# Kernel tuning notes

Hardware: AMD Instinct MI355X
Metric: run time of the kernel (lower is better)

Reference implementation:

```python
import jax, jax.numpy as jnp
import numpy as np

INPUT_DIM = 23
LSTM_DIM = 128
HID = 64            # lstm_dim // 2 per direction
MAMBA_DIM = 128
D_INNER = 256       # expand * d_model
D_STATE = 64
D_CONV = 4
DT_RANK = 8         # ceil(d_model / 16)
NUM_LAYERS = 4
SEQ, BATCH = 2048, 4


def setup_inputs() -> dict:
    key = jax.random.key(0)
    ks = iter(jax.random.split(key, 40))
    def rn(shape, s=0.05):
        return jax.random.normal(next(ks), shape, jnp.float32) * s
    inp = {}
    inp["x"] = jax.random.normal(next(ks), (SEQ, BATCH, INPUT_DIM), jnp.float32)
    # 4-layer bidirectional LSTM params (PyTorch layout: W_ih [4H, in], W_hh [4H, H])
    inp["lstm_Wih0"] = rn((2, 4 * HID, INPUT_DIM))
    inp["lstm_WihR"] = rn((NUM_LAYERS - 1, 2, 4 * HID, LSTM_DIM))
    inp["lstm_Whh"] = rn((NUM_LAYERS, 2, 4 * HID, HID))
    inp["lstm_bih"] = rn((NUM_LAYERS, 2, 4 * HID))
    inp["lstm_bhh"] = rn((NUM_LAYERS, 2, 4 * HID))
    # mamba input projection Linear(input_dim, mamba_dim)
    inp["mproj_W"] = rn((MAMBA_DIM, INPUT_DIM))
    inp["mproj_b"] = rn((MAMBA_DIM,))
    # Mamba block params
    inp["in_proj_W"] = rn((2 * D_INNER, MAMBA_DIM))
    inp["conv_w"] = rn((D_INNER, 1, D_CONV))
    inp["conv_b"] = rn((D_INNER,))
    inp["x_proj_W"] = rn((DT_RANK + 2 * D_STATE, D_INNER))
    inp["dt_W"] = rn((D_INNER, DT_RANK))
    inp["dt_b"] = rn((D_INNER,))
    inp["A_log"] = jnp.tile(jnp.log(jnp.arange(1.0, D_STATE + 1.0, dtype=jnp.float32))[None, :], (D_INNER, 1))
    inp["D_skip"] = jnp.ones((D_INNER,), jnp.float32)
    inp["out_proj_W"] = rn((MAMBA_DIM, D_INNER))
    # gate: LayerNorm(lstm_dim + mamba_dim) -> Linear(-> 1) -> sigmoid
    inp["gate_ln_w"] = jnp.ones((LSTM_DIM + MAMBA_DIM,), jnp.float32)
    inp["gate_ln_b"] = jnp.zeros((LSTM_DIM + MAMBA_DIM,), jnp.float32)
    inp["gate_W"] = rn((1, LSTM_DIM + MAMBA_DIM))
    inp["gate_b"] = rn((1,))
    return inp


def _lstm_dir(x, Wih, Whh, b, reverse):
    # x: [L, B, in]; one direction of one LSTM layer. PyTorch gate order i,f,g,o.
    h0 = jnp.zeros((x.shape[1], Whh.shape[1]), x.dtype)
    def step(carry, xt):
        h, c = carry
        g = xt @ Wih.T + h @ Whh.T + b
        i, f, gg, o = jnp.split(g, 4, axis=-1)
        c = jax.nn.sigmoid(f) * c + jax.nn.sigmoid(i) * jnp.tanh(gg)
        h = jax.nn.sigmoid(o) * jnp.tanh(c)
        return (h, c), h
    _, hs = jax.lax.scan(step, (h0, h0), x, reverse=reverse)
    return hs


def _lstm(x, Wih0, WihR, Whh, bih, bhh):
    out = x
    for l in range(NUM_LAYERS):
        Wf = Wih0[0] if l == 0 else WihR[l - 1, 0]
        Wb = Wih0[1] if l == 0 else WihR[l - 1, 1]
        hf = _lstm_dir(out, Wf, Whh[l, 0], bih[l, 0] + bhh[l, 0], False)
        hb = _lstm_dir(out, Wb, Whh[l, 1], bih[l, 1] + bhh[l, 1], True)
        out = jnp.concatenate([hf, hb], axis=-1)  # [L, B, 2H]
    return out


def _mamba(x, in_proj_W, conv_w, conv_b, x_proj_W, dt_W, dt_b, A_log, D_skip, out_proj_W):
    # x: [L, B, d_model]; time axis = 0
    L = x.shape[0]
    xi, z = jnp.split(x @ in_proj_W.T, 2, axis=-1)          # [L,B,d_inner] each
    xp = jnp.pad(xi, ((D_CONV - 1, 0), (0, 0), (0, 0)))      # causal depthwise conv
    conv = conv_b + sum(xp[k:k + L] * conv_w[:, 0, k] for k in range(D_CONV))
    xc = jax.nn.silu(conv)
    dbc = xc @ x_proj_W.T                                    # [L,B,dt_rank+2*d_state]
    dt, Bm, Cm = jnp.split(dbc, [DT_RANK, DT_RANK + D_STATE], axis=-1)
    dt = jax.nn.softplus(dt @ dt_W.T + dt_b)                 # [L,B,d_inner]
    A = -jnp.exp(A_log)                                      # [d_inner,d_state]
    def step(h, inp):
        dt_t, B_t, C_t, x_t = inp
        h = jnp.exp(dt_t[..., None] * A) * h + dt_t[..., None] * B_t[:, None, :] * x_t[..., None]
        return h, jnp.einsum('bds,bs->bd', h, C_t)
    h0 = jnp.zeros((x.shape[1], D_INNER, D_STATE), x.dtype)
    _, ys = jax.lax.scan(step, h0, (dt, Bm, Cm, xc))          # ys: [L,B,d_inner]
    y = (ys + xc * D_skip) * jax.nn.silu(z)
    return y @ out_proj_W.T                                   # [L,B,d_model]


def _forward(x, lstm_Wih0, lstm_WihR, lstm_Whh, lstm_bih, lstm_bhh, mproj_W, mproj_b,
             in_proj_W, conv_w, conv_b, x_proj_W, dt_W, dt_b, A_log, D_skip, out_proj_W,
             gate_ln_w, gate_ln_b, gate_W, gate_b):
    lstm_out = _lstm(x, lstm_Wih0, lstm_WihR, lstm_Whh, lstm_bih, lstm_bhh)  # [L,B,128]
    mamba_out = _mamba(x @ mproj_W.T + mproj_b, in_proj_W, conv_w, conv_b,
                       x_proj_W, dt_W, dt_b, A_log, D_skip, out_proj_W)      # [L,B,128]
    comb = jnp.concatenate([lstm_out, mamba_out], axis=-1)                   # [L,B,256]
    mu = comb.mean(-1, keepdims=True)
    var = comb.var(-1, keepdims=True)
    ln = (comb - mu) / jnp.sqrt(var + 1e-5) * gate_ln_w + gate_ln_b
    gate = jax.nn.sigmoid(ln @ gate_W.T + gate_b)                            # [L,B,1]
    return gate * lstm_out + (1.0 - gate) * mamba_out


def reference(x, lstm_Wih0, lstm_WihR, lstm_Whh, lstm_bih, lstm_bhh, mproj_W, mproj_b,
              in_proj_W, conv_w, conv_b, x_proj_W, dt_W, dt_b, A_log, D_skip, out_proj_W,
              gate_ln_w, gate_ln_b, gate_W, gate_b):
    return _forward(x, lstm_Wih0, lstm_WihR, lstm_Whh, lstm_bih, lstm_bhh, mproj_W, mproj_b,
                    in_proj_W, conv_w, conv_b, x_proj_W, dt_W, dt_b, A_log, D_skip, out_proj_W,
                    gate_ln_w, gate_ln_b, gate_W, gate_b)
```

## Files before the change

### kernel.cpp

```cpp
#include <hip/hip_runtime.h>

#define SEQ   2048
#define NM    8192

typedef __attribute__((ext_vector_type(4))) float f4;
typedef _Float16 f16x8 __attribute__((ext_vector_type(8)));

__device__ __forceinline__ float frcp(float x){ return __builtin_amdgcn_rcpf(x); }
__device__ __forceinline__ float sigm(float x){ return frcp(1.f + __expf(-x)); }
__device__ __forceinline__ float tanhf_(float x){ return 1.f - 2.f*frcp(__expf(2.f*x) + 1.f); }
__device__ __forceinline__ f4 mfma16h(f16x8 a, f16x8 b, f4 c){
  return __builtin_amdgcn_mfma_f32_16x16x32_f16(a, b, c, 0, 0, 0);
}
__device__ __forceinline__ void barrier_lds_only(){
  asm volatile("s_waitcnt lgkmcnt(0)\n\ts_barrier" ::: "memory");
}

__global__ __launch_bounds__(256) void gemm_k(
    const float* __restrict__ A, int lda,
    const float* __restrict__ W0, const float* __restrict__ W1, int Nhalf,
    const float* __restrict__ b0a, const float* __restrict__ b0b,
    const float* __restrict__ b1a, const float* __restrict__ b1b,
    float* __restrict__ out, int M, int N, int K, int mode)
{
  __shared__ alignas(16) float As[16][68];
  __shared__ alignas(16) float Ws[16][68];
  const int tid = threadIdx.x;
  const int tn = tid & 15, tm = tid >> 4;
  const int n0 = blockIdx.x * 64, m0 = blockIdx.y * 64;
  const int srow = tid >> 2, sk = (tid & 3) * 4;
  float acc[4][4] = {};
  for (int k0 = 0; k0 < K; k0 += 16) {
    const int am = m0 + srow;
    #pragma unroll
    for (int q = 0; q < 4; ++q) {
      int k = k0 + sk + q;
      As[sk + q][srow] = (k < K) ? A[(size_t)am * lda + k] : 0.f;
    }
    const int wn = n0 + srow;
    const float* Wp = W0; int nn = wn;
    if (W1 != nullptr && wn >= Nhalf) { Wp = W1; nn = wn - Nhalf; }
    #pragma unroll
    for (int q = 0; q < 4; ++q) {
      int k = k0 + sk + q;
      Ws[sk + q][srow] = (wn < N && k < K) ? Wp[(size_t)nn * K + k] : 0.f;
    }
    __syncthreads();
    #pragma unroll
    for (int k = 0; k < 16; ++k) {
      f4 a = *(const f4*)&As[k][tm*4];
      f4 w = *(const f4*)&Ws[k][tn*4];
      #pragma unroll
      for (int i = 0; i < 4; ++i)
        #pragma unroll
        for (int j = 0; j < 4; ++j) acc[i][j] += a[i]*w[j];
    }
    __syncthreads();
  }
  #pragma unroll
  for (int i = 0; i < 4; ++i) {
    #pragma unroll
    for (int j = 0; j < 4; ++j) {
      int m = m0 + tm*4 + i, n = n0 + tn*4 + j;
      if (n >= N) continue;
      float bias = 0.f;
      if (n < Nhalf) { if (b0a) bias += b0a[n]; if (b0b) bias += b0b[n]; }
      else { if (b1a) bias += b1a[n - Nhalf]; if (b1b) bias += b1b[n - Nhalf]; }
      float v = acc[i][j] + bias;
      if (mode == 2) {
        int dd = n >> 8, r = n & 255, t = m >> 2, b = m & 3;
        int gate = r >> 6, jj = r & 63;
        int tq = dd ? (SEQ - 1 - t) : t;
        out[((size_t)(dd*SEQ + tq) * 4 + b) * 256 + (jj << 2) + gate] = v;
      } else {
        out[(size_t)m * N + n] = v;
      }
    }
  }
}

__global__ __launch_bounds__(256) void wcomb_k(
    const float* __restrict__ inprojW, const float* __restrict__ mprojW,
    const float* __restrict__ mprojB, float* __restrict__ wc,
    float* __restrict__ bvec)
{
  int idx = blockIdx.x * 256 + threadIdx.x;
  if (idx >= 512 * 24) return;
  int n = idx / 24, c = idx % 24;
  const float* wi = inprojW + (size_t)n * 128;
  float s = 0.f;
  if (c < 23) {
    for (int k = 0; k < 128; ++k) s += wi[k] * mprojW[k*23 + c];
    wc[n*23 + c] = s;
  } else {
    for (int k = 0; k < 128; ++k) s += wi[k] * mprojB[k];
    bvec[n] = s;
  }
}

__global__ __launch_bounds__(256) void moutproj_k(
    const float* __restrict__ z, const float* __restrict__ ys,
    const float* __restrict__ xc, const float* __restrict__ Dsk,
    const float* __restrict__ Wp, float* __restrict__ out)
{
  __shared__ alignas(16) float As[16][68];
  __shared__ alignas(16) float Ws[16][68];
  const int tid = threadIdx.x;
  const int tn = tid & 15, tm = tid >> 4;
  const int n0 = blockIdx.x * 64, m0 = blockIdx.y * 64;
  const int srow = tid >> 2, sk = (tid & 3) * 4;
  float acc[4][4] = {};
  for (int k0 = 0; k0 < 256; k0 += 16) {
    #pragma unroll
    for (int q = 0; q < 4; ++q) {
      int k = k0 + sk + q;
      size_t idx = (size_t)(m0 + srow) * 256 + k;
      float zz = z[idx];
      As[sk + q][srow] = (ys[idx] + xc[idx]*Dsk[k]) * zz * sigm(zz);
      Ws[sk + q][srow] = Wp[(size_t)(n0 + srow) * 256 + k];
    }
    __syncthreads();
    #pragma unroll
    for (int k = 0; k < 16; ++k) {
      f4 a = *(const f4*)&As[k][tm*4];
      f4 w = *(const f4*)&Ws[k][tn*4];
      #pragma unroll
      for (int i = 0; i < 4; ++i)
        #pragma unroll
        for (int j = 0; j < 4; ++j) acc[i][j] += a[i]*w[j];
    }
    __syncthreads();
  }
  #pragma unroll
  for (int i = 0; i < 4; ++i)
    #pragma unroll
    for (int j = 0; j < 4; ++j)
      out[(size_t)(m0 + tm*4 + i) * 128 + n0 + tn*4 + j] = acc[i][j];
}

__global__ __launch_bounds__(256, 1) void fused_k(
    int stage,
    const float* __restrict__ G,
    const float* __restrict__ Whh,
    float* __restrict__ lout,
    const float* __restrict__ rA, int lda,
    const float* __restrict__ rW, const float* __restrict__ rbias,
    float* __restrict__ rout, int ldo, int N, int K,
    const float* __restrict__ dtW, const float* __restrict__ dtB,
    float* __restrict__ dtout,
    const float* __restrict__ mdbc, const float* __restrict__ mdtb,
    const float* __restrict__ mxc, const float* __restrict__ mAlog,
    float* __restrict__ mys)
{
  __shared__ alignas(16) _Float16 hb2[2][4][80];
  __shared__ float As[64][17];
  __shared__ float Ws[64][17];
  __shared__ float dtl[64][8];

  const int tid = threadIdx.x;

  if (blockIdx.x < 2) {
    __builtin_amdgcn_s_setprio(1);
    const int dir = blockIdx.x;
    const int w = tid >> 6, lane = tid & 63;
    const int q = lane >> 4, c = lane & 15;
    const int bb = c & 3, sel = c >> 2;
    const int mtile = 4*sel + w;
    const int jcol = mtile*4 + q;

    for (int i = tid; i < 2*4*80; i += 256) ((_Float16*)hb2)[i] = (_Float16)0.f;

    const float* Gd = G + (size_t)dir * SEQ * 1024;
    const float* Wd = Whh + dir * 256 * 64;

    f16x8 Wf[4][2];
    #pragma unroll
    for (int s2 = 0; s2 < 4; ++s2) {
      const int m = 4*s2 + w;
      const int orow = (c & 3)*64 + m*4 + (c >> 2);
      #pragma unroll
      for (int kt = 0; kt < 2; ++kt) {
        const float* src = Wd + orow*64 + kt*32 + q*8;
        #pragma unroll
        for (int e = 0; e < 8; ++e) Wf[s2][kt][e] = (_Float16)src[e];
      }
    }

    float cc = 0.f;

    auto loadG = [&](int t) -> f4 {
      return *(const f4*)(Gd + (((size_t)t*4 + bb) << 8) + mtile*16 + q*4);
    };
    f4 gp[8];
    #pragma unroll
    for (int i = 0; i < 8; ++i) gp[i] = loadG(i);
    __syncthreads();

    const bool sb0 = (sel & 1) != 0, sb1 = (sel & 2) != 0;

    auto step = [&](int t, f4 gv) {
      const int p0 = t & 1, p1 = p0 ^ 1;
      const f16x8 h0 = *(const f16x8*)&hb2[p0][bb][q*8];
      const f16x8 h1 = *(const f16x8*)&hb2[p0][bb][32 + q*8];
      const f4 zz = {0.f, 0.f, 0.f, 0.f};
      f4 a0 = mfma16h(Wf[0][0], h0, gv);
      f4 b0 = mfma16h(Wf[0][1], h1, zz);
      f4 a1 = mfma16h(Wf[1][0], h0, gv);
      f4 b1 = mfma16h(Wf[1][1], h1, zz);
      f4 a2 = mfma16h(Wf[2][0], h0, gv);
      f4 b2 = mfma16h(Wf[2][1], h1, zz);
      f4 a3 = mfma16h(Wf[3][0], h0, gv);
      f4 b3 = mfma16h(Wf[3][1], h1, zz);
      f4 g4;
      #pragma unroll
      for (int r = 0; r < 4; ++r) {
        float xlo01 = sb0 ? a1[r] : a0[r];
        float xlo23 = sb0 ? a3[r] : a2[r];
        float xlo   = sb1 ? xlo23 : xlo01;
        float xhi01 = sb0 ? b1[r] : b0[r];
        float xhi23 = sb0 ? b3[r] : b2[r];
        float xhi   = sb1 ? xhi23 : xhi01;
        g4[r] = xlo + xhi;
      }
      cc = sigm(g4[1])*cc + sigm(g4[0])*tanhf_(g4[2]);
      const float hh = sigm(g4[3])*tanhf_(cc);
      hb2[p1][bb][jcol] = (_Float16)hh;
      const int to = dir ? (SEQ-1 - t) : t;
      lout[((size_t)to*4 + bb)*128 + dir*64 + jcol] = hh;
      barrier_lds_only();
    };

    for (int t0 = 0; t0 < SEQ; t0 += 8) {
      #pragma unroll
      for (int i = 0; i < 8; ++i) {
        step(t0 + i, gp[i]);
        if (t0 + 8 + i < SEQ) gp[i] = loadG(t0 + 8 + i);
      }
    }
    return;
  }

  int rb = blockIdx.x - 2;

  if (stage == 1) {
    int idx = rb*256 + tid;
    int d = idx & 255, m2 = idx >> 8;
    int t = m2 >> 2, b = m2 & 3;
    float s = rbias[d];
    #pragma unroll
    for (int k = 0; k < 4; ++k) {
      int tt = t - 3 + k;
      if (tt >= 0) s += rA[(size_t)((tt*4 + b) << 8) + d] * rW[d*4 + k];
    }
    rout[idx] = s * sigm(s);
    return;
  }

  if (stage == 3) {
    const int wid = rb*4 + (tid >> 6);
    const int lane = tid & 63;
    const int b = wid >> 8, d = wid & 255;
    const float Av = -__expf(mAlog[d*64 + lane]);
    const float* pB  = mdbc + (size_t)b*136 + 8 + lane;
    const float* pC  = mdbc + (size_t)b*136 + 72 + lane;
    const float* pdt = mdtb + (size_t)b*256 + d;
    const float* px  = mxc  + (size_t)b*256 + d;
    float* py = mys + (size_t)b*256 + d;
    float h = 0.f;
    float Bv = pB[0], Cv = pC[0], dtv = pdt[0], xv = px[0];
    #pragma unroll 2
    for (int t = 0; t < SEQ; ++t) {
      float Bn = 0.f, Cn = 0.f, dtn = 0.f, xn = 0.f;
      if (t + 1 < SEQ) {
        size_t od = (size_t)(t+1) * 544;
        size_t ox = (size_t)(t+1) * 1024;
        Bn = pB[od]; Cn = pC[od]; dtn = pdt[ox]; xn = px[ox];
      }
      float a = __expf(dtv * Av);
      h = a*h + (dtv*xv)*Bv;
      float p = h * Cv;
      #pragma unroll
      for (int mm = 1; mm < 64; mm <<= 1) p += __shfl_xor(p, mm, 64);
      if (lane == 0) py[(size_t)t * 1024] = p;
      Bv = Bn; Cv = Cn; dtv = dtn; xv = xn;
    }
    return;
  }

  const float* gW = rW; const float* gB = rbias; float* gO = rout;
  if (stage == 0 && rb >= 512) { rb -= 512; gW = dtW; gB = dtB; gO = dtout; }
  const int ntiles = (N + 63) >> 6;
  const int nt = rb % ntiles, mt = rb / ntiles;
  const int n0 = nt * 64, m0 = mt * 64;
  const int tn = tid & 15, tm = tid >> 4;
  const int srow = tid >> 2, sk = (tid & 3) * 4;
  float acc[4][4] = {};
  for (int k0 = 0; k0 < K; k0 += 16) {
    #pragma unroll
    for (int qq = 0; qq < 4; ++qq) {
      int k = k0 + sk + qq;
      As[srow][sk + qq] = (k < K) ? rA[(size_t)(m0 + srow) * lda + k] : 0.f;
      Ws[srow][sk + qq] = (n0 + srow < N && k < K) ? gW[(size_t)(n0 + srow) * K + k] : 0.f;
    }
    __syncthreads();
    #pragma unroll
    for (int k = 0; k < 16; ++k) {
      float a[4], w[4];
      #pragma unroll
      for (int i = 0; i < 4; ++i) a[i] = As[tm*4+i][k];
      #pragma unroll
      for (int j = 0; j < 4; ++j) w[j] = Ws[tn*4+j][k];
      #pragma unroll
      for (int i = 0; i < 4; ++i)
        #pragma unroll
        for (int j = 0; j < 4; ++j) acc[i][j] += a[i]*w[j];
    }
    __syncthreads();
  }
  #pragma unroll
  for (int i = 0; i < 4; ++i) {
    #pragma unroll
    for (int j = 0; j < 4; ++j) {
      int m2 = m0 + tm*4 + i, n = n0 + tn*4 + j;
      if (n >= N) continue;
      float v = acc[i][j] + (gB ? gB[n] : 0.f);
      gO[(size_t)m2 * ldo + n] = v;
      if (stage == 2 && nt == 0 && n < 8) dtl[tm*4+i][n] = v;
    }
  }
  if (stage == 2 && nt == 0) {
    __syncthreads();
    for (int idx = tid; idx < 64*256; idx += 256) {
      int ml = idx >> 8, d = idx & 255;
      float s = dtB[d];
      #pragma unroll
      for (int r = 0; r < 8; ++r) s += dtl[ml][r] * dtW[d*8 + r];
      s = (s > 15.f) ? s : __logf(1.f + __expf(s));
      dtout[(size_t)(m0 + ml)*256 + d] = s;
    }
  }
}

__global__ __launch_bounds__(256) void combine_k(
    const float* __restrict__ lstm, const float* __restrict__ mam,
    const float* __restrict__ lnw, const float* __restrict__ lnb,
    const float* __restrict__ gW, const float* __restrict__ gb,
    float* __restrict__ out)
{
  const int pair = blockIdx.x * 4 + (threadIdx.x >> 6);
  const int lane = threadIdx.x & 63;
  const float2 lv = *(const float2*)(lstm + (size_t)pair*128 + lane*2);
  const float2 mv = *(const float2*)(mam  + (size_t)pair*128 + lane*2);
  float s  = lv.x + lv.y + mv.x + mv.y;
  float sq = lv.x*lv.x + lv.y*lv.y + mv.x*mv.x + mv.y*mv.y;
  #pragma unroll
  for (int mm = 1; mm < 64; mm <<= 1) { s += __shfl_xor(s, mm, 64); sq += __shfl_xor(sq, mm, 64); }
  const float mean = s * (1.f/256.f);
  const float var  = sq * (1.f/256.f) - mean*mean;
  const float inv  = rsqrtf(var + 1e-5f);
  const int c0 = lane*2, c2 = 128 + lane*2;
  float n0 = (lv.x-mean)*inv*lnw[c0]   + lnb[c0];
  float n1 = (lv.y-mean)*inv*lnw[c0+1] + lnb[c0+1];
  float n2 = (mv.x-mean)*inv*lnw[c2]   + lnb[c2];
  float n3 = (mv.y-mean)*inv*lnw[c2+1] + lnb[c2+1];
  float dot = n0*gW[c0] + n1*gW[c0+1] + n2*gW[c2] + n3*gW[c2+1];
  #pragma unroll
  for (int mm = 1; mm < 64; mm <<= 1) dot += __shfl_xor(dot, mm, 64);
  const float gate = sigm(dot + gb[0]);
  float2 o;
  o.x = gate*lv.x + (1.f-gate)*mv.x;
  o.y = gate*lv.y + (1.f-gate)*mv.y;
  *(float2*)(out + (size_t)pair*128 + lane*2) = o;
}

extern "C" void kernel_launch(void* const* d_in, const int* in_sizes, int n_in,
                              void* d_out, int out_size, void* d_ws, size_t ws_size,
                              hipStream_t stream)
{
  const float* x       = (const float*)d_in[0];
  const float* Wih0    = (const float*)d_in[1];
  const float* WihR    = (const float*)d_in[2];
  const float* Whh     = (const float*)d_in[3];
  const float* bih     = (const float*)d_in[4];
  const float* bhh     = (const float*)d_in[5];
  const float* mprojW  = (const float*)d_in[6];
  const float* mprojB  = (const float*)d_in[7];
  const float* inprojW = (const float*)d_in[8];
  const float* convw   = (const float*)d_in[9];
  const float* convb   = (const float*)d_in[10];
  const float* xprojW  = (const float*)d_in[11];
  const float* dtW     = (const float*)d_in[12];
  const float* dtB     = (const float*)d_in[13];
  const float* Alog    = (const float*)d_in[14];
  const float* Dskip   = (const float*)d_in[15];
  const float* outprojW= (const float*)d_in[16];
  const float* lnw     = (const float*)d_in[17];
  const float* lnb     = (const float*)d_in[18];
  const float* gWt     = (const float*)d_in[19];
  const float* gb      = (const float*)d_in[20];

  float* WS = (float*)d_ws;
  const size_t M1 = 1048576;
  float* mamba_out = WS;
  float* P     = WS + M1;
  float* G     = P;
  float* lstmA = P + 4*M1;
  float* lstmB = P + 5*M1;
  float* xi    = P + 6*M1;
  float* dtb   = P + 6*M1;
  float* xc    = P + 8*M1;
  float* dbc   = P + 10*M1;
  float* wc    = P + 10*M1 + (size_t)NM*136;
  float* bvec  = wc + 512*23;
  float* ysb   = P + 11*M1 + M1/4;
  const bool zOK = ws_size >= 65ull*1048576;
  float* zbuf  = zOK ? (P + 13*M1 + M1/4)
                     : (P + 6*M1);
  float* outp  = (float*)d_out;

  dim3 blk(256);

  wcomb_k<<<48, blk, 0, stream>>>(inprojW, mprojW, mprojB, wc, bvec);

  const float* lin = x;
  float* louts[4] = {lstmA, lstmB, lstmA, lstmB};
  for (int l = 0; l < 4; ++l) {
    const float* w0; const float* w1; int K;
    if (l == 0) { w0 = Wih0; w1 = Wih0 + 256*23; K = 23; }
    else {
      w0 = WihR + (size_t)((l-1)*2 + 0)*256*128;
      w1 = WihR + (size_t)((l-1)*2 + 1)*256*128;
      K = 128;
    }
    gemm_k<<<dim3(8,128), blk, 0, stream>>>(lin, K, w0, w1, 256,
        bih + (l*2+0)*256, bhh + (l*2+0)*256,
        bih + (l*2+1)*256, bhh + (l*2+1)*256,
        G, NM, 512, K, 2);
    const float* Wl = Whh + (size_t)l*2*256*64;
    if (l == 0) {
      fused_k<<<2 + (zOK ? 1024 : 512), blk, 0, stream>>>(0, G, Wl, louts[l],
          x, 23, wc, bvec, xi, 256, 256, 23,
          zOK ? (wc + 256*23) : nullptr, zOK ? (bvec + 256) : nullptr,
          zOK ? zbuf : nullptr, nullptr, nullptr, nullptr, nullptr, nullptr);
    } else if (l == 1) {
      fused_k<<<2 + 8192, blk, 0, stream>>>(1, G, Wl, louts[l],
          xi, 0, convw, convb, xc, 0, 0, 0,
          nullptr, nullptr, nullptr, nullptr, nullptr, nullptr, nullptr, nullptr);
    } else if (l == 2) {
      fused_k<<<2 + 384, blk, 0, stream>>>(2, G, Wl, louts[l],
          xc, 256, xprojW, nullptr, dbc, 136, 136, 256,
          dtW, dtB, dtb, nullptr, nullptr, nullptr, nullptr, nullptr);
    } else {
      fused_k<<<2 + 256, blk, 0, stream>>>(3, G, Wl, louts[l],
          nullptr, 0, nullptr, nullptr, nullptr, 0, 0, 0,
          nullptr, nullptr, nullptr, dbc, dtb, xc, Alog, ysb);
    }
    lin = louts[l];
  }

  if (!zOK) {
    gemm_k<<<dim3(4,128), blk, 0, stream>>>(x, 23, wc + 256*23, nullptr, 256,
        bvec + 256, nullptr, nullptr, nullptr, zbuf, NM, 256, 23, 0);
  }
  moutproj_k<<<dim3(2,128), blk, 0, stream>>>(zbuf, ysb, xc, Dskip,
      outprojW, mamba_out);
  combine_k<<<2048, blk, 0, stream>>>(lstmB, mamba_out, lnw, lnb, gWt, gb, outp);
}
```

Measured before the change: 3.236 ms.

## Overlap next-layer LSTM input GEMM with current recurrence via progress counters

Removes the separate input-projection GEMM launches for LSTM layers 1-3. Extra blocks are appended to the current layer's fused kernel, and each one computes a tile of the next layer's gate preactivations. Before starting, a block spin-waits on per-direction progress counters that the recurrent blocks publish with release stores every 64 steps. This hides the GEMM and launch gaps behind the serial recurrence, at the cost of spin-waiting blocks that hold CU slots. It also depends on careful ordering, because these blocks write into the G buffer the recurrence is still reading.

```diff
diff --git a/kernel.cpp b/kernel.cpp
--- a/kernel.cpp
+++ b/kernel.cpp
@@ -81,20 +81,28 @@
 
 __global__ __launch_bounds__(256) void wcomb_k(
     const float* __restrict__ inprojW, const float* __restrict__ mprojW,
-    const float* __restrict__ mprojB, float* __restrict__ wc,
-    float* __restrict__ bvec)
+    const float* __restrict__ mprojB, const float* __restrict__ bih,
+    const float* __restrict__ bhh, float* __restrict__ wc,
+    float* __restrict__ bvec, float* __restrict__ bsum, int* cnt)
 {
   int idx = blockIdx.x * 256 + threadIdx.x;
-  if (idx >= 512 * 24) return;
-  int n = idx / 24, c = idx % 24;
-  const float* wi = inprojW + (size_t)n * 128;
-  float s = 0.f;
-  if (c < 23) {
-    for (int k = 0; k < 128; ++k) s += wi[k] * mprojW[k*23 + c];
-    wc[n*23 + c] = s;
-  } else {
-    for (int k = 0; k < 128; ++k) s += wi[k] * mprojB[k];
-    bvec[n] = s;
+  if (idx < 512 * 24) {
+    int n = idx / 24, c = idx % 24;
+    const float* wi = inprojW + (size_t)n * 128;
+    float s = 0.f;
+    if (c < 23) {
+      for (int k = 0; k < 128; ++k) s += wi[k] * mprojW[k*23 + c];
+      wc[n*23 + c] = s;
+    } else {
+      for (int k = 0; k < 128; ++k) s += wi[k] * mprojB[k];
+      bvec[n] = s;
+    }
+  } else if (idx < 512*24 + 1536) {
+    int j = idx - 512*24;
+    bsum[j] = bih[512 + j] + bhh[512 + j];
+  } else if (idx < 512*24 + 1536 + 8) {
+    __hip_atomic_store(&cnt[idx - (512*24 + 1536)], 0,
+                       __ATOMIC_RELEASE, __HIP_MEMORY_SCOPE_AGENT);
   }
 }
 
@@ -150,7 +158,9 @@
     float* __restrict__ dtout,
     const float* __restrict__ mdbc, const float* __restrict__ mdtb,
     const float* __restrict__ mxc, const float* __restrict__ mAlog,
-    float* __restrict__ mys)
+    float* __restrict__ mys,
+    const float* nA, const float* nW0, const float* nW1,
+    const float* nb, float* nG, int* cnt, int firstG)
 {
   __shared__ alignas(16) _Float16 hb2[2][4][80];
   __shared__ float As[64][17];
@@ -236,11 +246,90 @@
         step(t0 + i, gp[i]);
         if (t0 + 8 + i < SEQ) gp[i] = loadG(t0 + 8 + i);
       }
+      if (cnt != nullptr && ((t0 & 63) == 56)) {
+        asm volatile("s_waitcnt vmcnt(0)" ::: "memory");
+        __syncthreads();
+        if (tid == 0)
+          __hip_atomic_store(&cnt[dir], t0 + 7,
+                             __ATOMIC_RELEASE, __HIP_MEMORY_SCOPE_AGENT);
+      }
+    }
+    if (cnt != nullptr) {
+      asm volatile("s_waitcnt vmcnt(0)" ::: "memory");
+      __syncthreads();
+      if (tid == 0)
+        __hip_atomic_store(&cnt[dir], SEQ,
+                           __ATOMIC_RELEASE, __HIP_MEMORY_SCOPE_AGENT);
     }
     return;
   }
 
   int rb = blockIdx.x - 2;
+
+  if (nW0 != nullptr && rb >= firstG) {
+    const int g  = rb - firstG;
+    const int mt = g >> 1, nh = g & 1;
+    const int T0 = mt * 16;
+    const int need0 = T0 + 16;
+    const int need1 = SEQ - 1 - T0;
+    if (tid == 0) {
+      while (__hip_atomic_fetch_add(&cnt[0], 0,
+               __ATOMIC_RELAXED, __HIP_MEMORY_SCOPE_AGENT) < need0)
+        __builtin_amdgcn_s_sleep(127);
+      while (__hip_atomic_fetch_add(&cnt[1], 0,
+               __ATOMIC_RELAXED, __HIP_MEMORY_SCOPE_AGENT) < need1)
+        __builtin_amdgcn_s_sleep(127);
+      (void)__hip_atomic_load(&cnt[0], __ATOMIC_ACQUIRE,
+                              __HIP_MEMORY_SCOPE_AGENT);
+    }
+    __syncthreads();
+    const int tn = tid & 15, tm = tid >> 4;
+    const int srow = tid >> 2, sk = (tid & 3) * 4;
+    const int m0g = mt * 64;
+    const int wn = 0;  (void)wn;
+    for (int ntl = 0; ntl < 4; ++ntl) {
+      const int n0g = (nh*4 + ntl) * 64;
+      const int wrow = n0g + srow;
+      const float* Wp = (wrow < 256) ? nW0 : nW1;
+      const int nn = (wrow < 256) ? wrow : wrow - 256;
+      float acc[4][4] = {};
+      for (int k0 = 0; k0 < 128; k0 += 16) {
+        #pragma unroll
+        for (int qq = 0; qq < 4; ++qq) {
+          int k = k0 + sk + qq;
+          As[srow][sk + qq] = nA[(size_t)(m0g + srow) * 128 + k];
+          Ws[srow][sk + qq] = Wp[(size_t)nn * 128 + k];
+        }
+        __syncthreads();
+        #pragma unroll
+        for (int k = 0; k < 16; ++k) {
+          float a[4], wv[4];
+          #pragma unroll
+          for (int i = 0; i < 4; ++i) a[i] = As[tm*4+i][k];
+          #pragma unroll
+          for (int j = 0; j < 4; ++j) wv[j] = Ws[tn*4+j][k];
+          #pragma unroll
+          for (int i = 0; i < 4; ++i)
+            #pragma unroll
+            for (int j = 0; j < 4; ++j) acc[i][j] += a[i]*wv[j];
+        }
+        __syncthreads();
+      }
+      #pragma unroll
+      for (int i = 0; i < 4; ++i) {
+        #pragma unroll
+        for (int j = 0; j < 4; ++j) {
+          int m = m0g + tm*4 + i, n = n0g + tn*4 + j;
+          float v = acc[i][j] + nb[n];
+          int dd = n >> 8, r2 = n & 255, t = m >> 2, b = m & 3;
+          int gate = r2 >> 6, jj = r2 & 63;
+          int tq = dd ? (SEQ - 1 - t) : t;
+          nG[((size_t)(dd*SEQ + tq) * 4 + b) * 256 + (jj << 2) + gate] = v;
+        }
+      }
+    }
+    return;
+  }
 
   if (stage == 1) {
     int idx = rb*256 + tid;
@@ -412,6 +501,8 @@
   float* dbc   = P + 10*M1;
   float* wc    = P + 10*M1 + (size_t)NM*136;
   float* bvec  = wc + 512*23;
+  float* bsum  = bvec + 512;
+  int*   cntB  = (int*)(bsum + 1536);
   float* ysb   = P + 11*M1 + M1/4;
   const bool zOK = ws_size >= 65ull*1048576;
   float* zbuf  = zOK ? (P + 13*M1 + M1/4)
@@ -420,40 +511,46 @@
 
   dim3 blk(256);
 
-  wcomb_k<<<48, blk, 0, stream>>>(inprojW, mprojW, mprojB, wc, bvec);
+  wcomb_k<<<55, blk, 0, stream>>>(inprojW, mprojW, mprojB, bih, bhh,
+                                  wc, bvec, bsum, cntB);
 
   const float* lin = x;
   float* louts[4] = {lstmA, lstmB, lstmA, lstmB};
   for (int l = 0; l < 4; ++l) {
-    const float* w0; const float* w1; int K;
-    if (l == 0) { w0 = Wih0; w1 = Wih0 + 256*23; K = 23; }
-    else {
-      w0 = WihR + (size_t)((l-1)*2 + 0)*256*128;
-      w1 = WihR + (size_t)((l-1)*2 + 1)*256*128;
-      K = 128;
-    }
-    gemm_k<<<dim3(8,128), blk, 0, stream>>>(lin, K, w0, w1, 256,
-        bih + (l*2+0)*256, bhh + (l*2+0)*256,
-        bih + (l*2+1)*256, bhh + (l*2+1)*256,
-        G, NM, 512, K, 2);
+    if (l == 0) {
+      gemm_k<<<dim3(8,128), blk, 0, stream>>>(x, 23, Wih0, Wih0 + 256*23, 256,
+          bih + 0*256, bhh + 0*256, bih + 1*256, bhh + 1*256,
+          G, NM, 512, 23, 2);
+    }
     const float* Wl = Whh + (size_t)l*2*256*64;
+    const bool hasG = (l < 3);
+    const float* nW0 = hasG ? (WihR + (size_t)(l*2 + 0)*256*128) : nullptr;
+    const float* nW1 = hasG ? (WihR + (size_t)(l*2 + 1)*256*128) : nullptr;
+    const float* nbp = hasG ? (bsum + (size_t)l*512) : nullptr;
+    int* cntp = hasG ? (cntB + 2*l) : nullptr;
+
     if (l == 0) {
-      fused_k<<<2 + (zOK ? 1024 : 512), blk, 0, stream>>>(0, G, Wl, louts[l],
+      int firstG = zOK ? 1024 : 512;
+      fused_k<<<2 + firstG + 256, blk, 0, stream>>>(0, G, Wl, louts[l],
           x, 23, wc, bvec, xi, 256, 256, 23,
           zOK ? (wc + 256*23) : nullptr, zOK ? (bvec + 256) : nullptr,
-          zOK ? zbuf : nullptr, nullptr, nullptr, nullptr, nullptr, nullptr);
+          zOK ? zbuf : nullptr, nullptr, nullptr, nullptr, nullptr, nullptr,
+          louts[l], nW0, nW1, nbp, G, cntp, firstG);
     } else if (l == 1) {
-      fused_k<<<2 + 8192, blk, 0, stream>>>(1, G, Wl, louts[l],
+      fused_k<<<2 + 8192 + 256, blk, 0, stream>>>(1, G, Wl, louts[l],
           xi, 0, convw, convb, xc, 0, 0, 0,
-          nullptr, nullptr, nullptr, nullptr, nullptr, nullptr, nullptr, nullptr);
+          nullptr, nullptr, nullptr, nullptr, nullptr, nullptr, nullptr, nullptr,
+          louts[l], nW0, nW1, nbp, G, cntp, 8192);
     } else if (l == 2) {
-      fused_k<<<2 + 384, blk, 0, stream>>>(2, G, Wl, louts[l],
+      fused_k<<<2 + 384 + 256, blk, 0, stream>>>(2, G, Wl, louts[l],
           xc, 256, xprojW, nullptr, dbc, 136, 136, 256,
-          dtW, dtB, dtb, nullptr, nullptr, nullptr, nullptr, nullptr);
+          dtW, dtB, dtb, nullptr, nullptr, nullptr, nullptr, nullptr,
+          louts[l], nW0, nW1, nbp, G, cntp, 384);
     } else {
       fused_k<<<2 + 256, blk, 0, stream>>>(3, G, Wl, louts[l],
           nullptr, 0, nullptr, nullptr, nullptr, 0, 0, 0,
-          nullptr, nullptr, nullptr, dbc, dtb, xc, Alog, ysb);
+          nullptr, nullptr, nullptr, dbc, dtb, xc, Alog, ysb,
+          nullptr, nullptr, nullptr, nullptr, nullptr, nullptr, 0);
     }
     lin = louts[l];
   }
```

Result: no change. 3.257 ms (+0.7%).
